# Kernel tuning notes

Measured on AMD Instinct MI355X. Metric: run time of the kernel, lower is better.

## Reference

```python
import jax, jax.numpy as jnp
import numpy as np
import math

B, S, E, H = 2, 2048, 1024, 16
D = E // H
EPS = 1e-5


def setup_inputs() -> dict:
    key = jax.random.key(0)
    ks = jax.random.split(key, 6)
    s = 1.0 / math.sqrt(E)
    return {
        "query": jax.random.normal(ks[0], (B, S, E), jnp.float32),
        "Wq": jax.random.normal(ks[1], (E, E), jnp.float32) * s,
        "bq": jnp.zeros((E,), jnp.float32),
        "Wk": jax.random.normal(ks[2], (E, E), jnp.float32) * s,
        "bk": jnp.zeros((E,), jnp.float32),
        "Wv": jax.random.normal(ks[3], (E, E), jnp.float32) * s,
        "bv": jnp.zeros((E,), jnp.float32),
        "Wo": jax.random.normal(ks[4], (E, E), jnp.float32) * s,
        "bo": jnp.zeros((E,), jnp.float32),
        "alpha": jnp.ones((1,), jnp.float32),
    }


def reference(query, Wq, bq, Wk, bk, Wv, bv, Wo, bo, alpha):
    # Q/K/V projections (nn.Linear: x @ W.T + b)
    q = (query @ Wq.T + bq).reshape(B, S, H, D)
    k = (query @ Wk.T + bk).reshape(B, S, H, D)
    v = (query @ Wv.T + bv).reshape(B, S, H, D)

    # YAT scores: (q.k)^2 / (||q-k||^2 + eps)
    qk = jnp.einsum('bqhd,bkhd->bhqk', q, k)          # [B,H,S,S]
    sq = jnp.einsum('bqhd,bqhd->bhq', q, q)           # ||q||^2
    sk = jnp.einsum('bkhd,bkhd->bhk', k, k)           # ||k||^2
    dist_sq = sq[..., :, None] + sk[..., None, :] - 2.0 * qk
    scores = (qk * qk) / (dist_sq + EPS)

    # learnable alpha scaling: scores * (sqrt(d)/log(1+d))^alpha
    scale = (jnp.sqrt(jnp.float32(D)) / jnp.log1p(jnp.float32(D))) ** alpha[0]
    scores = scores * scale

    attn = jax.nn.softmax(scores, axis=-1)
    out = jnp.einsum('bhqk,bkhd->bqhd', attn, v).reshape(B, S, E)
    return out @ Wo.T + bo
```

## Files before the change

### kernel.cpp

```cpp
#include <hip/hip_runtime.h>
#include <hip/hip_fp16.h>
#include <math.h>

#define BB 2
#define SS 2048
#define EE 1024
#define HH 16
#define DD 64
#define YAT_EPS 1e-5f
#define RR (BB * HH * SS)

typedef __attribute__((ext_vector_type(8))) short bf16x8;
typedef __attribute__((ext_vector_type(4))) short short4v;
typedef __attribute__((ext_vector_type(4))) float f32x4;
#define MFMA16(a, b, c) __builtin_amdgcn_mfma_f32_16x16x32_bf16((a), (b), (c), 0, 0, 0)

#if __has_builtin(__builtin_amdgcn_exp2f)
#define EXP2(x) __builtin_amdgcn_exp2f(x)
#else
#define EXP2(x) exp2f(x)
#endif
#if __has_builtin(__builtin_amdgcn_rcpf)
#define RCPF(x) __builtin_amdgcn_rcpf(x)
#else
#define RCPF(x) (1.0f / (x))
#endif

__device__ __forceinline__ unsigned short f2bf(float x) {
    unsigned int u = __float_as_uint(x);
    u += 0x7FFFu + ((u >> 16) & 1u);
    return (unsigned short)(u >> 16);
}
__device__ __forceinline__ float bf2f(unsigned short h) {
    return __uint_as_float(((unsigned int)h) << 16);
}

__device__ __forceinline__ void async_ld16(void* lds, const void* g) {
    __builtin_amdgcn_global_load_lds(
        (const __attribute__((address_space(1))) unsigned int*)g,
        (__attribute__((address_space(3))) unsigned int*)lds, 16, 0, 0);
}

__global__ __launch_bounds__(256) void split_f32(const float* __restrict__ in,
                                                 unsigned short* __restrict__ hi,
                                                 unsigned short* __restrict__ lo,
                                                 int n4) {
    int i = blockIdx.x * 256 + threadIdx.x;
    if (i >= n4) return;
    float4 v = ((const float4*)in)[i];
    ushort4 h, l;
    h.x = f2bf(v.x); l.x = f2bf(v.x - bf2f(h.x));
    h.y = f2bf(v.y); l.y = f2bf(v.y - bf2f(h.y));
    h.z = f2bf(v.z); l.z = f2bf(v.z - bf2f(h.z));
    h.w = f2bf(v.w); l.w = f2bf(v.w - bf2f(h.w));
    ((ushort4*)hi)[i] = h;
    ((ushort4*)lo)[i] = l;
}

template <int MODE>
__global__ __launch_bounds__(256, 2) void gemm3p(
        const unsigned short* __restrict__ Ahi, const unsigned short* __restrict__ Alo,
        const unsigned short* __restrict__ Bhi, const unsigned short* __restrict__ Blo,
        const float* __restrict__ bq, const float* __restrict__ bk,
        const float* __restrict__ bv,
        float* __restrict__ Cf,
        unsigned short* __restrict__ qhi, unsigned short* __restrict__ qlo,
        unsigned short* __restrict__ khi, unsigned short* __restrict__ klo,
        unsigned short* __restrict__ v_sd,
        float* __restrict__ sqn, float* __restrict__ skn,
        int M, int N, int K) {
    __shared__ __align__(16) unsigned short LA_hi[128 * 32];
    __shared__ __align__(16) unsigned short LA_lo[128 * 32];
    __shared__ __align__(16) unsigned short LB_hi[128 * 32];
    __shared__ __align__(16) unsigned short LB_lo[128 * 32];

    const int t = threadIdx.x;
    const int w = t >> 6, lane = t & 63;
    const int quad = lane >> 4, lr = lane & 15;
    const int wy = w & 1, wx = w >> 1;
    const int m0 = blockIdx.y * 128, n0 = blockIdx.x * 128;

    const unsigned short* gsrc;
    unsigned short* ldst;
    if (w == 0)      { gsrc = Ahi + (size_t)m0 * K; ldst = LA_hi; }
    else if (w == 1) { gsrc = Alo + (size_t)m0 * K; ldst = LA_lo; }
    else if (w == 2) { gsrc = Bhi + (size_t)n0 * K; ldst = LB_hi; }
    else             { gsrc = Blo + (size_t)n0 * K; ldst = LB_lo; }
    const unsigned short* gl = gsrc + (size_t)(lane >> 2) * K + (lane & 3) * 8;

    f32x4 acc[4][4];
    #pragma unroll
    for (int i = 0; i < 4; ++i)
        #pragma unroll
        for (int j = 0; j < 4; ++j)
            acc[i][j] = (f32x4){0.f, 0.f, 0.f, 0.f};

    for (int k0 = 0; k0 < K; k0 += 32) {
        __syncthreads();
        #pragma unroll
        for (int i = 0; i < 8; ++i)
            async_ld16(ldst + i * 512, gl + (size_t)i * 16 * K + k0);
        __syncthreads();
        bf16x8 ah[4], al[4], bh_[4], bl_[4];
        #pragma unroll
        for (int i = 0; i < 4; ++i) {
            ah[i]  = *(const bf16x8*)&LA_hi[(wy * 64 + i * 16 + lr) * 32 + quad * 8];
            al[i]  = *(const bf16x8*)&LA_lo[(wy * 64 + i * 16 + lr) * 32 + quad * 8];
            bh_[i] = *(const bf16x8*)&LB_hi[(wx * 64 + i * 16 + lr) * 32 + quad * 8];
            bl_[i] = *(const bf16x8*)&LB_lo[(wx * 64 + i * 16 + lr) * 32 + quad * 8];
        }
        #pragma unroll
        for (int mg = 0; mg < 4; ++mg)
            #pragma unroll
            for (int ns = 0; ns < 4; ++ns) {
                f32x4 a = acc[mg][ns];
                a = MFMA16(ah[mg], bh_[ns], a);
                a = MFMA16(ah[mg], bl_[ns], a);
                a = MFMA16(al[mg], bh_[ns], a);
                acc[mg][ns] = a;
            }
    }

    const int ng = n0 + wx * 64;
    if (MODE == 0) {
        float bias_v[4];
        #pragma unroll
        for (int ns = 0; ns < 4; ++ns) bias_v[ns] = bq[ng + ns * 16 + lr];
        #pragma unroll
        for (int mg = 0; mg < 4; ++mg)
            #pragma unroll
            for (int r = 0; r < 4; ++r) {
                int m = m0 + wy * 64 + mg * 16 + quad * 4 + r;
                #pragma unroll
                for (int ns = 0; ns < 4; ++ns)
                    Cf[(size_t)m * N + ng + ns * 16 + lr] = acc[mg][ns][r] + bias_v[ns];
            }
    } else {
        const int path = ng >> 10;
        const int c = ng & 1023;
        const int h = c >> 6;
        const float* bias = path == 0 ? bq : path == 1 ? bk : bv;
        unsigned short* hi_p = path == 0 ? qhi : khi;
        unsigned short* lo_p = path == 0 ? qlo : klo;
        float* nrm = path == 0 ? sqn : skn;
        float bias_v[4];
        #pragma unroll
        for (int ns = 0; ns < 4; ++ns) bias_v[ns] = bias[c + ns * 16 + lr];
        #pragma unroll
        for (int mg = 0; mg < 4; ++mg)
            #pragma unroll
            for (int r = 0; r < 4; ++r) {
                int m = m0 + wy * 64 + mg * 16 + quad * 4 + r;
                int b = m >> 11, s = m & (SS - 1);
                size_t base = ((size_t)(b * HH + h) * SS + s) * DD;
                float v4[4];
                #pragma unroll
                for (int ns = 0; ns < 4; ++ns) v4[ns] = acc[mg][ns][r] + bias_v[ns];
                if (path < 2) {
                    float pn = v4[0] * v4[0] + v4[1] * v4[1] + v4[2] * v4[2] + v4[3] * v4[3];
                    #pragma unroll
                    for (int off = 1; off < 16; off <<= 1) pn += __shfl_xor(pn, off);
                    if (lr == 0) nrm[(size_t)(b * HH + h) * SS + s] = pn;
                    #pragma unroll
                    for (int ns = 0; ns < 4; ++ns) {
                        unsigned short hv = f2bf(v4[ns]);
                        hi_p[base + ns * 16 + lr] = hv;
                        lo_p[base + ns * 16 + lr] = f2bf(v4[ns] - bf2f(hv));
                    }
                } else {
                    #pragma unroll
                    for (int ns = 0; ns < 4; ++ns)
                        v_sd[base + ns * 16 + lr] = f2bf(v4[ns]);
                }
            }
    }
}

__global__ __launch_bounds__(256) void transpose_v(const unsigned short* __restrict__ v_sd,
                                                   unsigned short* __restrict__ vt) {
    __shared__ unsigned short T[64][65];
    const int t = threadIdx.x;
    const int bh = blockIdx.y, s0 = blockIdx.x * 64;
    {
        int sl = t >> 2, d4 = (t & 3) * 16;
        const unsigned short* src = &v_sd[((size_t)bh * SS + s0 + sl) * DD + d4];
        bf16x8 a = *(const bf16x8*)src;
        bf16x8 b = *(const bf16x8*)(src + 8);
        #pragma unroll
        for (int j = 0; j < 8; ++j) {
            T[sl][d4 + j] = (unsigned short)a[j];
            T[sl][d4 + 8 + j] = (unsigned short)b[j];
        }
    }
    __syncthreads();
    {
        int dl = t >> 2, s4 = (t & 3) * 16;
        bf16x8 a, b;
        #pragma unroll
        for (int j = 0; j < 8; ++j) {
            a[j] = (short)T[s4 + j][dl];
            b[j] = (short)T[s4 + 8 + j][dl];
        }
        unsigned short* dst = &vt[((size_t)bh * DD + dl) * SS + s0 + s4];
        *(bf16x8*)dst = a;
        *(bf16x8*)(dst + 8) = b;
    }
}

__global__ __launch_bounds__(256, 3) void yat_attn_mfma(
        const unsigned short* __restrict__ qhi, const unsigned short* __restrict__ qlo,
        const unsigned short* __restrict__ khi, const unsigned short* __restrict__ klo,
        const unsigned short* __restrict__ vt,
        const float* __restrict__ sqn, const float* __restrict__ skn,
        const float* __restrict__ alphap,
        __half* __restrict__ Opart, float2* __restrict__ mlpart) {
    __shared__ __align__(16) unsigned short Ks[2][8192];
    __shared__ __align__(16) unsigned short Ps[4][2][16 * 68];

    const int t = threadIdx.x;
    const int w = t >> 6, lane = t & 63;
    const int quad = lane >> 4, lr = lane & 15;
    const int qt = blockIdx.x, bh = blockIdx.y, z = blockIdx.z;
    const int row0 = qt * 128 + w * 32;
    const float cscale = powf(sqrtf((float)DD) / log1pf((float)DD), alphap[0])
                         * 1.4426950408889634f;

    bf16x8 qh[2][2], ql[2][2];
    float sqe[2];
    #pragma unroll
    for (int mg = 0; mg < 2; ++mg) {
        #pragma unroll
        for (int kd = 0; kd < 2; ++kd) {
            size_t o = ((size_t)bh * SS + row0 + mg * 16 + lr) * DD + kd * 32 + quad * 8;
            qh[mg][kd] = *(const bf16x8*)&qhi[o];
            ql[mg][kd] = *(const bf16x8*)&qlo[o];
        }
        sqe[mg] = sqn[(size_t)bh * SS + row0 + mg * 16 + lr] + YAT_EPS;
    }

    const int lrow = lane >> 3;
    const int lofs = lrow * 64 + (((lane & 7) ^ (lrow & 7)) << 3);

    float m_r[2] = {-INFINITY, -INFINITY}, l_r[2] = {0.f, 0.f};
    f32x4 O[2][4];
    #pragma unroll
    for (int mg = 0; mg < 2; ++mg)
        #pragma unroll
        for (int nd = 0; nd < 4; ++nd) O[mg][nd] = (f32x4){0.f, 0.f, 0.f, 0.f};

    const int kt0 = z * 16;
    {
        const size_t gbase = ((size_t)bh * SS + kt0 * 64 + w * 16) * 64 + lofs;
        #pragma unroll
        for (int i2 = 0; i2 < 2; ++i2) {
            async_ld16(&Ks[0][w * 1024 + i2 * 512],        khi + gbase + i2 * 512);
            async_ld16(&Ks[0][4096 + w * 1024 + i2 * 512], klo + gbase + i2 * 512);
        }
    }

    for (int it = 0; it < 16; ++it) {
        const int kt = kt0 + it;
        const int p = it & 1;
        const int kbase = kt * 64;
        __syncthreads();
        if (it < 15) {
            const size_t gbase = ((size_t)bh * SS + (kt + 1) * 64 + w * 16) * 64 + lofs;
            #pragma unroll
            for (int i2 = 0; i2 < 2; ++i2) {
                async_ld16(&Ks[p ^ 1][w * 1024 + i2 * 512],        khi + gbase + i2 * 512);
                async_ld16(&Ks[p ^ 1][4096 + w * 1024 + i2 * 512], klo + gbase + i2 * 512);
            }
        }
        f32x4 acc[2][4];
        f32x4 sk4[4];
        const unsigned short* kb = Ks[p];
        const int sw = lr & 7;
        #pragma unroll
        for (int st = 0; st < 4; ++st) {
            const int rbase = (st * 16 + lr) * 64;
            bf16x8 kh0 = *(const bf16x8*)&kb[rbase + ((quad    ) ^ sw) * 8];
            bf16x8 kh1 = *(const bf16x8*)&kb[rbase + ((quad + 4) ^ sw) * 8];
            bf16x8 kl0 = *(const bf16x8*)&kb[4096 + rbase + ((quad    ) ^ sw) * 8];
            bf16x8 kl1 = *(const bf16x8*)&kb[4096 + rbase + ((quad + 4) ^ sw) * 8];
            sk4[st] = *(const f32x4*)&skn[(size_t)bh * SS + kbase + st * 16 + quad * 4];
            #pragma unroll
            for (int mg = 0; mg < 2; ++mg) {
                f32x4 a = (f32x4){0.f, 0.f, 0.f, 0.f};
                a = MFMA16(kh0, qh[mg][0], a);
                a = MFMA16(kh1, qh[mg][1], a);
                a = MFMA16(kl0, qh[mg][0], a);
                a = MFMA16(kl1, qh[mg][1], a);
                a = MFMA16(kh0, ql[mg][0], a);
                a = MFMA16(kh1, ql[mg][1], a);
                acc[mg][st] = a;
            }
        }
        bf16x8 vf[4][2];
        #pragma unroll
        for (int nd = 0; nd < 4; ++nd)
            #pragma unroll
            for (int kk = 0; kk < 2; ++kk)
                vf[nd][kk] = *(const bf16x8*)&vt[((size_t)bh * DD + nd * 16 + lr) * SS
                                                 + kbase + kk * 32 + quad * 8];
        #pragma unroll
        for (int mg = 0; mg < 2; ++mg) {
            unsigned short* myP = Ps[w][mg];
            float mx = -INFINITY;
            #pragma unroll
            for (int st = 0; st < 4; ++st)
                #pragma unroll
                for (int r = 0; r < 4; ++r) {
                    float qk = acc[mg][st][r];
                    float d = sqe[mg] + sk4[st][r] - 2.f * qk;
                    float s = qk * qk * cscale * RCPF(d);
                    acc[mg][st][r] = s;
                    mx = fmaxf(mx, s);
                }
            mx = fmaxf(mx, __shfl_xor(mx, 16));
            mx = fmaxf(mx, __shfl_xor(mx, 32));
            float mnew = fmaxf(m_r[mg], mx);
            float aa = EXP2(m_r[mg] - mnew);
            m_r[mg] = mnew;
            float rs = 0.f;
            #pragma unroll
            for (int st = 0; st < 4; ++st)
                #pragma unroll
                for (int r = 0; r < 4; ++r) {
                    float e = EXP2(acc[mg][st][r] - mnew);
                    acc[mg][st][r] = e;
                    rs += e;
                }
            rs += __shfl_xor(rs, 16);
            rs += __shfl_xor(rs, 32);
            l_r[mg] = l_r[mg] * aa + rs;
            #pragma unroll
            for (int st = 0; st < 4; ++st) {
                short4v pv;
                pv[0] = (short)f2bf(acc[mg][st][0]);
                pv[1] = (short)f2bf(acc[mg][st][1]);
                pv[2] = (short)f2bf(acc[mg][st][2]);
                pv[3] = (short)f2bf(acc[mg][st][3]);
                *(short4v*)&myP[lr * 68 + st * 16 + quad * 4] = pv;
            }
            float al_[4];
            #pragma unroll
            for (int r = 0; r < 4; ++r) al_[r] = __shfl(aa, quad * 4 + r);
            #pragma unroll
            for (int nd = 0; nd < 4; ++nd)
                #pragma unroll
                for (int r = 0; r < 4; ++r)
                    O[mg][nd][r] *= al_[r];
        }
        #pragma unroll
        for (int mg = 0; mg < 2; ++mg) {
            unsigned short* myP = Ps[w][mg];
            bf16x8 pf[2];
            #pragma unroll
            for (int kk = 0; kk < 2; ++kk)
                pf[kk] = *(const bf16x8*)&myP[lr * 68 + kk * 32 + quad * 8];
            #pragma unroll
            for (int nd = 0; nd < 4; ++nd)
                #pragma unroll
                for (int kk = 0; kk < 2; ++kk)
                    O[mg][nd] = MFMA16(pf[kk], vf[nd][kk], O[mg][nd]);
        }
    }
    #pragma unroll
    for (int mg = 0; mg < 2; ++mg) {
        if (quad == 0)
            mlpart[(size_t)z * RR + (size_t)bh * SS + row0 + mg * 16 + lr] =
                make_float2(m_r[mg], l_r[mg]);
        #pragma unroll
        for (int r = 0; r < 4; ++r) {
            size_t rowg = (size_t)bh * SS + row0 + mg * 16 + quad * 4 + r;
            #pragma unroll
            for (int nd = 0; nd < 4; ++nd)
                Opart[((size_t)z * RR + rowg) * DD + nd * 16 + lr] =
                    __float2half(O[mg][nd][r]);
        }
    }
}

__global__ __launch_bounds__(256) void combine_attn(
        const __half* __restrict__ Opart, const float2* __restrict__ mlpart,
        unsigned short* __restrict__ ctxhi, unsigned short* __restrict__ ctxlo) {
    int tid = blockIdx.x * 256 + threadIdx.x;
    int row = tid >> 4, c4 = (tid & 15) * 4;
    float2 ml0 = mlpart[row];
    float2 ml1 = mlpart[RR + row];
    float ms = fmaxf(ml0.x, ml1.x);
    float a0 = EXP2(ml0.x - ms), a1 = EXP2(ml1.x - ms);
    float inv = RCPF(ml0.y * a0 + ml1.y * a1);
    a0 *= inv; a1 *= inv;
    const __half* p0 = Opart + (size_t)row * DD + c4;
    const __half* p1 = p0 + (size_t)RR * DD;
    int bh = row >> 11, s = row & (SS - 1);
    int b = bh >> 4, h = bh & 15;
    size_t idx = ((size_t)b * SS + s) * EE + h * DD + c4;
    ushort4 hv, lv;
    unsigned short* hp = (unsigned short*)&hv;
    unsigned short* lp = (unsigned short*)&lv;
    #pragma unroll
    for (int j = 0; j < 4; ++j) {
        float o = __half2float(p0[j]) * a0 + __half2float(p1[j]) * a1;
        unsigned short hh = f2bf(o);
        hp[j] = hh;
        lp[j] = f2bf(o - bf2f(hh));
    }
    *(ushort4*)&ctxhi[idx] = hv;
    *(ushort4*)&ctxlo[idx] = lv;
}

extern "C" void kernel_launch(void* const* d_in, const int* in_sizes, int n_in,
                              void* d_out, int out_size, void* d_ws, size_t ws_size,
                              hipStream_t stream) {
    const float* x     = (const float*)d_in[0];
    const float* Wq    = (const float*)d_in[1];
    const float* bq    = (const float*)d_in[2];
    const float* Wk    = (const float*)d_in[3];
    const float* bk    = (const float*)d_in[4];
    const float* Wv    = (const float*)d_in[5];
    const float* bv    = (const float*)d_in[6];
    const float* Wo    = (const float*)d_in[7];
    const float* bo    = (const float*)d_in[8];
    const float* alpha = (const float*)d_in[9];
    float* out = (float*)d_out;
    char* ws = (char*)d_ws;

    const int M = BB * SS;
    const size_t MB = 1u << 20;
    unsigned short* xhi  = (unsigned short*)(ws + 0 * MB);
    unsigned short* xlo  = (unsigned short*)(ws + 8 * MB);
    unsigned short* Whi  = (unsigned short*)(ws + 16 * MB);
    unsigned short* Wlo  = (unsigned short*)(ws + 22 * MB);
    unsigned short* vt   = (unsigned short*)(ws + 16 * MB);
    float2* mlpart       = (float2*)(ws + 24 * MB);
    unsigned short* Wohi = (unsigned short*)(ws + 28 * MB);
    unsigned short* Wolo = (unsigned short*)(ws + 30 * MB);
    unsigned short* qhi  = (unsigned short*)(ws + 32 * MB);
    unsigned short* qlo  = (unsigned short*)(ws + 40 * MB);
    unsigned short* khi  = (unsigned short*)(ws + 48 * MB);
    unsigned short* klo  = (unsigned short*)(ws + 56 * MB);
    unsigned short* v_sd = (unsigned short*)(ws + 64 * MB);
    __half* Opart        = (__half*)(ws + 64 * MB);
    float* sqn = (float*)(ws + 80 * MB);
    float* skn = (float*)(ws + 80 * MB + 256 * 1024);
    unsigned short* ctxhi = xhi;
    unsigned short* ctxlo = xlo;

    const int nX = M * EE / 4, nW = EE * EE / 4;
    split_f32<<<nX / 256, 256, 0, stream>>>(x, xhi, xlo, nX);
    split_f32<<<nW / 256, 256, 0, stream>>>(Wq, Whi, Wlo, nW);
    split_f32<<<nW / 256, 256, 0, stream>>>(Wk, Whi + (size_t)EE * EE, Wlo + (size_t)EE * EE, nW);
    split_f32<<<nW / 256, 256, 0, stream>>>(Wv, Whi + 2 * (size_t)EE * EE, Wlo + 2 * (size_t)EE * EE, nW);
    split_f32<<<nW / 256, 256, 0, stream>>>(Wo, Wohi, Wolo, nW);

    gemm3p<1><<<dim3(3 * EE / 128, M / 128), 256, 0, stream>>>(
        xhi, xlo, Whi, Wlo, bq, bk, bv, nullptr,
        qhi, qlo, khi, klo, v_sd, sqn, skn, M, 3 * EE, EE);

    transpose_v<<<dim3(SS / 64, BB * HH), 256, 0, stream>>>(v_sd, vt);

    yat_attn_mfma<<<dim3(SS / 128, BB * HH, 2), 256, 0, stream>>>(
        qhi, qlo, khi, klo, vt, sqn, skn, alpha, Opart, mlpart);

    combine_attn<<<RR * 16 / 256, 256, 0, stream>>>(Opart, mlpart, ctxhi, ctxlo);

    gemm3p<0><<<dim3(EE / 128, M / 128), 256, 0, stream>>>(
        ctxhi, ctxlo, Wohi, Wolo, bo, nullptr, nullptr, out,
        nullptr, nullptr, nullptr, nullptr, nullptr, nullptr, nullptr, M, EE, EE);
}
```

Measured before the change: 385.3 us.

## Halve attention query tile per wave, double-buffer P, and fuse weight splits

The attention kernel now gives each wave 16 query rows instead of 32, so blocks cover 64 rows and the grid doubles. The P scratch buffer is double-buffered by iteration parity. The four per-weight split launches are merged into a single 2D-grid kernel. Smaller tiles cut register pressure and add blocks for occupancy, but each K tile loaded into LDS and each V fragment loaded from global memory is now reused over half as many query rows, doubling K/V traffic.

```diff
diff --git a/kernel.cpp b/kernel.cpp
--- a/kernel.cpp
+++ b/kernel.cpp
@@ -48,6 +48,26 @@
     int i = blockIdx.x * 256 + threadIdx.x;
     if (i >= n4) return;
     float4 v = ((const float4*)in)[i];
+    ushort4 h, l;
+    h.x = f2bf(v.x); l.x = f2bf(v.x - bf2f(h.x));
+    h.y = f2bf(v.y); l.y = f2bf(v.y - bf2f(h.y));
+    h.z = f2bf(v.z); l.z = f2bf(v.z - bf2f(h.z));
+    h.w = f2bf(v.w); l.w = f2bf(v.w - bf2f(h.w));
+    ((ushort4*)hi)[i] = h;
+    ((ushort4*)lo)[i] = l;
+}
+
+__global__ __launch_bounds__(256) void split_w4(
+        const float* __restrict__ Wq, const float* __restrict__ Wk,
+        const float* __restrict__ Wv, const float* __restrict__ Wo,
+        unsigned short* __restrict__ Whi, unsigned short* __restrict__ Wlo,
+        unsigned short* __restrict__ Wohi, unsigned short* __restrict__ Wolo) {
+    int i = blockIdx.x * 256 + threadIdx.x;
+    int y = blockIdx.y;
+    const float* src = y == 0 ? Wq : y == 1 ? Wk : y == 2 ? Wv : Wo;
+    unsigned short* hi = y < 3 ? Whi + (size_t)y * EE * EE : Wohi;
+    unsigned short* lo = y < 3 ? Wlo + (size_t)y * EE * EE : Wolo;
+    float4 v = ((const float4*)src)[i];
     ushort4 h, l;
     h.x = f2bf(v.x); l.x = f2bf(v.x - bf2f(h.x));
     h.y = f2bf(v.y); l.y = f2bf(v.y - bf2f(h.y));
@@ -215,38 +235,32 @@
         const float* __restrict__ alphap,
         __half* __restrict__ Opart, float2* __restrict__ mlpart) {
     __shared__ __align__(16) unsigned short Ks[2][8192];
-    __shared__ __align__(16) unsigned short Ps[4][2][16 * 68];
+    __shared__ __align__(16) unsigned short Ps[2][4][16 * 68];
 
     const int t = threadIdx.x;
     const int w = t >> 6, lane = t & 63;
     const int quad = lane >> 4, lr = lane & 15;
     const int qt = blockIdx.x, bh = blockIdx.y, z = blockIdx.z;
-    const int row0 = qt * 128 + w * 32;
+    const int row0 = qt * 64 + w * 16;
     const float cscale = powf(sqrtf((float)DD) / log1pf((float)DD), alphap[0])
                          * 1.4426950408889634f;
 
-    bf16x8 qh[2][2], ql[2][2];
-    float sqe[2];
+    bf16x8 qh[2], ql[2];
     #pragma unroll
-    for (int mg = 0; mg < 2; ++mg) {
-        #pragma unroll
-        for (int kd = 0; kd < 2; ++kd) {
-            size_t o = ((size_t)bh * SS + row0 + mg * 16 + lr) * DD + kd * 32 + quad * 8;
-            qh[mg][kd] = *(const bf16x8*)&qhi[o];
-            ql[mg][kd] = *(const bf16x8*)&qlo[o];
-        }
-        sqe[mg] = sqn[(size_t)bh * SS + row0 + mg * 16 + lr] + YAT_EPS;
-    }
+    for (int kd = 0; kd < 2; ++kd) {
+        size_t o = ((size_t)bh * SS + row0 + lr) * DD + kd * 32 + quad * 8;
+        qh[kd] = *(const bf16x8*)&qhi[o];
+        ql[kd] = *(const bf16x8*)&qlo[o];
+    }
+    const float sqe = sqn[(size_t)bh * SS + row0 + lr] + YAT_EPS;
 
     const int lrow = lane >> 3;
     const int lofs = lrow * 64 + (((lane & 7) ^ (lrow & 7)) << 3);
 
-    float m_r[2] = {-INFINITY, -INFINITY}, l_r[2] = {0.f, 0.f};
-    f32x4 O[2][4];
+    float m_r = -INFINITY, l_r = 0.f;
+    f32x4 O[4];
     #pragma unroll
-    for (int mg = 0; mg < 2; ++mg)
-        #pragma unroll
-        for (int nd = 0; nd < 4; ++nd) O[mg][nd] = (f32x4){0.f, 0.f, 0.f, 0.f};
+    for (int nd = 0; nd < 4; ++nd) O[nd] = (f32x4){0.f, 0.f, 0.f, 0.f};
 
     const int kt0 = z * 16;
     {
@@ -271,7 +285,7 @@
                 async_ld16(&Ks[p ^ 1][4096 + w * 1024 + i2 * 512], klo + gbase + i2 * 512);
             }
         }
-        f32x4 acc[2][4];
+        f32x4 acc[4];
         f32x4 sk4[4];
         const unsigned short* kb = Ks[p];
         const int sw = lr & 7;
@@ -283,17 +297,14 @@
             bf16x8 kl0 = *(const bf16x8*)&kb[4096 + rbase + ((quad    ) ^ sw) * 8];
             bf16x8 kl1 = *(const bf16x8*)&kb[4096 + rbase + ((quad + 4) ^ sw) * 8];
             sk4[st] = *(const f32x4*)&skn[(size_t)bh * SS + kbase + st * 16 + quad * 4];
-            #pragma unroll
-            for (int mg = 0; mg < 2; ++mg) {
-                f32x4 a = (f32x4){0.f, 0.f, 0.f, 0.f};
-                a = MFMA16(kh0, qh[mg][0], a);
-                a = MFMA16(kh1, qh[mg][1], a);
-                a = MFMA16(kl0, qh[mg][0], a);
-                a = MFMA16(kl1, qh[mg][1], a);
-                a = MFMA16(kh0, ql[mg][0], a);
-                a = MFMA16(kh1, ql[mg][1], a);
-                acc[mg][st] = a;
-            }
+            f32x4 a = (f32x4){0.f, 0.f, 0.f, 0.f};
+            a = MFMA16(kh0, qh[0], a);
+            a = MFMA16(kh1, qh[1], a);
+            a = MFMA16(kl0, qh[0], a);
+            a = MFMA16(kl1, qh[1], a);
+            a = MFMA16(kh0, ql[0], a);
+            a = MFMA16(kh1, ql[1], a);
+            acc[st] = a;
         }
         bf16x8 vf[4][2];
         #pragma unroll
@@ -302,82 +313,71 @@
             for (int kk = 0; kk < 2; ++kk)
                 vf[nd][kk] = *(const bf16x8*)&vt[((size_t)bh * DD + nd * 16 + lr) * SS
                                                  + kbase + kk * 32 + quad * 8];
-        #pragma unroll
-        for (int mg = 0; mg < 2; ++mg) {
-            unsigned short* myP = Ps[w][mg];
-            float mx = -INFINITY;
-            #pragma unroll
-            for (int st = 0; st < 4; ++st)
-                #pragma unroll
-                for (int r = 0; r < 4; ++r) {
-                    float qk = acc[mg][st][r];
-                    float d = sqe[mg] + sk4[st][r] - 2.f * qk;
-                    float s = qk * qk * cscale * RCPF(d);
-                    acc[mg][st][r] = s;
-                    mx = fmaxf(mx, s);
-                }
-            mx = fmaxf(mx, __shfl_xor(mx, 16));
-            mx = fmaxf(mx, __shfl_xor(mx, 32));
-            float mnew = fmaxf(m_r[mg], mx);
-            float aa = EXP2(m_r[mg] - mnew);
-            m_r[mg] = mnew;
-            float rs = 0.f;
-            #pragma unroll
-            for (int st = 0; st < 4; ++st)
-                #pragma unroll
-                for (int r = 0; r < 4; ++r) {
-                    float e = EXP2(acc[mg][st][r] - mnew);
-                    acc[mg][st][r] = e;
-                    rs += e;
-                }
-            rs += __shfl_xor(rs, 16);
-            rs += __shfl_xor(rs, 32);
-            l_r[mg] = l_r[mg] * aa + rs;
-            #pragma unroll
-            for (int st = 0; st < 4; ++st) {
-                short4v pv;
-                pv[0] = (short)f2bf(acc[mg][st][0]);
-                pv[1] = (short)f2bf(acc[mg][st][1]);
-                pv[2] = (short)f2bf(acc[mg][st][2]);
-                pv[3] = (short)f2bf(acc[mg][st][3]);
-                *(short4v*)&myP[lr * 68 + st * 16 + quad * 4] = pv;
-            }
-            float al_[4];
-            #pragma unroll
-            for (int r = 0; r < 4; ++r) al_[r] = __shfl(aa, quad * 4 + r);
-            #pragma unroll
-            for (int nd = 0; nd < 4; ++nd)
-                #pragma unroll
-                for (int r = 0; r < 4; ++r)
-                    O[mg][nd][r] *= al_[r];
-        }
-        #pragma unroll
-        for (int mg = 0; mg < 2; ++mg) {
-            unsigned short* myP = Ps[w][mg];
-            bf16x8 pf[2];
+        unsigned short* myP = Ps[p][w];
+        float mx = -INFINITY;
+        #pragma unroll
+        for (int st = 0; st < 4; ++st)
+            #pragma unroll
+            for (int r = 0; r < 4; ++r) {
+                float qk = acc[st][r];
+                float d = sqe + sk4[st][r] - 2.f * qk;
+                float s = qk * qk * cscale * RCPF(d);
+                acc[st][r] = s;
+                mx = fmaxf(mx, s);
+            }
+        mx = fmaxf(mx, __shfl_xor(mx, 16));
+        mx = fmaxf(mx, __shfl_xor(mx, 32));
+        float mnew = fmaxf(m_r, mx);
+        float aa = EXP2(m_r - mnew);
+        m_r = mnew;
+        float rs = 0.f;
+        #pragma unroll
+        for (int st = 0; st < 4; ++st)
+            #pragma unroll
+            for (int r = 0; r < 4; ++r) {
+                float e = EXP2(acc[st][r] - mnew);
+                acc[st][r] = e;
+                rs += e;
+            }
+        rs += __shfl_xor(rs, 16);
+        rs += __shfl_xor(rs, 32);
+        l_r = l_r * aa + rs;
+        #pragma unroll
+        for (int st = 0; st < 4; ++st) {
+            short4v pv;
+            pv[0] = (short)f2bf(acc[st][0]);
+            pv[1] = (short)f2bf(acc[st][1]);
+            pv[2] = (short)f2bf(acc[st][2]);
+            pv[3] = (short)f2bf(acc[st][3]);
+            *(short4v*)&myP[lr * 68 + st * 16 + quad * 4] = pv;
+        }
+        float al_[4];
+        #pragma unroll
+        for (int r = 0; r < 4; ++r) al_[r] = __shfl(aa, quad * 4 + r);
+        #pragma unroll
+        for (int nd = 0; nd < 4; ++nd)
+            #pragma unroll
+            for (int r = 0; r < 4; ++r)
+                O[nd][r] *= al_[r];
+        bf16x8 pf[2];
+        #pragma unroll
+        for (int kk = 0; kk < 2; ++kk)
+            pf[kk] = *(const bf16x8*)&myP[lr * 68 + kk * 32 + quad * 8];
+        #pragma unroll
+        for (int nd = 0; nd < 4; ++nd)
             #pragma unroll
             for (int kk = 0; kk < 2; ++kk)
-                pf[kk] = *(const bf16x8*)&myP[lr * 68 + kk * 32 + quad * 8];
-            #pragma unroll
-            for (int nd = 0; nd < 4; ++nd)
-                #pragma unroll
-                for (int kk = 0; kk < 2; ++kk)
-                    O[mg][nd] = MFMA16(pf[kk], vf[nd][kk], O[mg][nd]);
-        }
-    }
+                O[nd] = MFMA16(pf[kk], vf[nd][kk], O[nd]);
+    }
+    if (quad == 0)
+        mlpart[(size_t)z * RR + (size_t)bh * SS + row0 + lr] = make_float2(m_r, l_r);
     #pragma unroll
-    for (int mg = 0; mg < 2; ++mg) {
-        if (quad == 0)
-            mlpart[(size_t)z * RR + (size_t)bh * SS + row0 + mg * 16 + lr] =
-                make_float2(m_r[mg], l_r[mg]);
-        #pragma unroll
-        for (int r = 0; r < 4; ++r) {
-            size_t rowg = (size_t)bh * SS + row0 + mg * 16 + quad * 4 + r;
-            #pragma unroll
-            for (int nd = 0; nd < 4; ++nd)
-                Opart[((size_t)z * RR + rowg) * DD + nd * 16 + lr] =
-                    __float2half(O[mg][nd][r]);
-        }
+    for (int r = 0; r < 4; ++r) {
+        size_t rowg = (size_t)bh * SS + row0 + quad * 4 + r;
+        #pragma unroll
+        for (int nd = 0; nd < 4; ++nd)
+            Opart[((size_t)z * RR + rowg) * DD + nd * 16 + lr] =
+                __float2half(O[nd][r]);
     }
 }
 
@@ -450,10 +450,8 @@
 
     const int nX = M * EE / 4, nW = EE * EE / 4;
     split_f32<<<nX / 256, 256, 0, stream>>>(x, xhi, xlo, nX);
-    split_f32<<<nW / 256, 256, 0, stream>>>(Wq, Whi, Wlo, nW);
-    split_f32<<<nW / 256, 256, 0, stream>>>(Wk, Whi + (size_t)EE * EE, Wlo + (size_t)EE * EE, nW);
-    split_f32<<<nW / 256, 256, 0, stream>>>(Wv, Whi + 2 * (size_t)EE * EE, Wlo + 2 * (size_t)EE * EE, nW);
-    split_f32<<<nW / 256, 256, 0, stream>>>(Wo, Wohi, Wolo, nW);
+    split_w4<<<dim3(nW / 256, 4), 256, 0, stream>>>(Wq, Wk, Wv, Wo,
+                                                    Whi, Wlo, Wohi, Wolo);
 
     gemm3p<1><<<dim3(3 * EE / 128, M / 128), 256, 0, stream>>>(
         xhi, xlo, Whi, Wlo, bq, bk, bv, nullptr,
@@ -461,7 +459,7 @@
 
     transpose_v<<<dim3(SS / 64, BB * HH), 256, 0, stream>>>(v_sd, vt);
 
-    yat_attn_mfma<<<dim3(SS / 128, BB * HH, 2), 256, 0, stream>>>(
+    yat_attn_mfma<<<dim3(SS / 64, BB * HH, 2), 256, 0, stream>>>(
         qhi, qlo, khi, klo, vt, sqn, skn, alpha, Opart, mlpart);
 
     combine_attn<<<RR * 16 / 256, 256, 0, stream>>>(Opart, mlpart, ctxhi, ctxlo);
```

After: 381.5 us. About the same (-1.0%).
